# Performance work log

Hardware: AMD Instinct MI355X
Metric: run time of the kernel (lower is better)

## Reference

```python
import jax, jax.numpy as jnp
import numpy as np

# Dims: T=out_seq_len, B=batch, D=hidden_dim, H=hidden_dim_de, E=embedding_size, C=feat_channels
T, B, D, H, E, C, FH, FW = 32, 16, 512, 512, 512, 512, 8, 32


def _lstm_dir(x_seq, W_ih, W_hh, b_ih, b_hh, reverse):
    # x_seq: (T, B, D); PyTorch gate order i, f, g, o
    gx = jnp.einsum('tbd,gd->tbg', x_seq, W_ih) + b_ih  # (T, B, 4H)
    Hh = W_hh.shape[1]
    def step(carry, g_t):
        h, c = carry
        g = g_t + h @ W_hh.T + b_hh
        i, f, gg, o = jnp.split(g, 4, axis=-1)
        c = jax.nn.sigmoid(f) * c + jax.nn.sigmoid(i) * jnp.tanh(gg)
        h = jax.nn.sigmoid(o) * jnp.tanh(c)
        return (h, c), h
    init = (jnp.zeros((x_seq.shape[1], Hh), x_seq.dtype),
            jnp.zeros((x_seq.shape[1], Hh), x_seq.dtype))
    _, hs = jax.lax.scan(step, init, gx, reverse=reverse)
    return hs  # (T, B, H)


def setup_inputs() -> dict:
    key = jax.random.key(0)
    ks = jax.random.split(key, 16)
    s = 0.02
    inp = {
        'hidden_en': jax.random.normal(ks[0], (T, B, D), jnp.float32),
        'conv_f': jax.random.normal(ks[1], (B, C, FH, FW), jnp.float32),
        # bidirectional LSTM params (PyTorch layout: W_ih (4H, D), W_hh (4H, H))
        'W_ih_f': jax.random.normal(ks[2], (4 * H, D), jnp.float32) * s,
        'W_hh_f': jax.random.normal(ks[3], (4 * H, H), jnp.float32) * s,
        'b_ih_f': jnp.zeros((4 * H,), jnp.float32),
        'b_hh_f': jnp.zeros((4 * H,), jnp.float32),
        'W_ih_b': jax.random.normal(ks[4], (4 * H, D), jnp.float32) * s,
        'W_hh_b': jax.random.normal(ks[5], (4 * H, H), jnp.float32) * s,
        'b_ih_b': jnp.zeros((4 * H,), jnp.float32),
        'b_hh_b': jnp.zeros((4 * H,), jnp.float32),
        # linear_decode: (H, 2H)
        'W_dec': jax.random.normal(ks[6], (H, 2 * H), jnp.float32) * s,
        'b_dec': jnp.zeros((H,), jnp.float32),
        # conv_em: 3x3, C -> E (OIHW)
        'W_em': jax.random.normal(ks[7], (E, C, 3, 3), jnp.float32) * s,
        'b_em': jnp.zeros((E,), jnp.float32),
        # attention h_em: 1x1 conv == linear H -> E
        'W_hem': jax.random.normal(ks[8], (E, H), jnp.float32) * s,
        'b_hem': jnp.zeros((E,), jnp.float32),
        # conv_att: 1x1 conv E -> 1
        'w_att': jax.random.normal(ks[9], (E,), jnp.float32) * s,
        'b_att': jnp.zeros((), jnp.float32),
    }
    return inp


def reference(hidden_en, conv_f, W_ih_f, W_hh_f, b_ih_f, b_hh_f,
              W_ih_b, W_hh_b, b_ih_b, b_hh_b, W_dec, b_dec,
              W_em, b_em, W_hem, b_hem, w_att, b_att):
    # decoder_ctc: bidirectional LSTM + linear
    h_fwd = _lstm_dir(hidden_en, W_ih_f, W_hh_f, b_ih_f, b_hh_f, reverse=False)
    h_bwd = _lstm_dir(hidden_en, W_ih_b, W_hh_b, b_ih_b, b_hh_b, reverse=True)
    hidden_de = jnp.concatenate([h_fwd, h_bwd], axis=-1) @ W_dec.T + b_dec  # (T, B, H)

    # conv_em: 3x3 same-padding conv, NCHW
    x_em = jax.lax.conv_general_dilated(
        conv_f, W_em, window_strides=(1, 1), padding='SAME',
        dimension_numbers=('NCHW', 'OIHW', 'NCHW')) + b_em[None, :, None, None]  # (B,E,FH,FW)
    att_x_em = jnp.transpose(x_em.reshape(x_em.shape[0], E, -1), (0, 2, 1))  # (B, HW, E)

    # batched attention over all timesteps (dropout is identity at eval)
    h_em = jnp.einsum('tbh,eh->tbe', hidden_de, W_hem) + b_hem  # (T, B, E)
    feat = jnp.tanh(x_em[None] + h_em[:, :, :, None, None])     # (T, B, E, FH, FW)
    scores = jnp.einsum('tbehw,e->tbhw', feat, w_att) + b_att   # (T, B, FH, FW)
    alpha = jax.nn.softmax(scores.reshape(scores.shape[0], scores.shape[1], -1), axis=-1)  # (T,B,HW)
    att = jnp.einsum('tbn,bne->tbe', alpha, att_x_em)           # (T, B, E)

    ctc_out = jnp.concatenate([hidden_de, att], axis=-1)        # (T, B, H+E)
    return jnp.transpose(ctc_out, (1, 0, 2))                    # (B, T, H+E)
```

## Files before the change

### kernel.cpp

```cpp
#include <hip/hip_runtime.h>
#include <hip/hip_bf16.h>
#include <math.h>

#define T_LEN 32
#define BATCH 16
#define DDIM  512
#define HDIM  512
#define EDIM  512
#define CDIM  512
#define FHH   8
#define FWW   32
#define HW    256
#define G4    2048
#define PADH  10
#define PADW  34
#define WLP   520

typedef __attribute__((ext_vector_type(8))) short bf16x8;
typedef __attribute__((ext_vector_type(4))) float f32x4;

__device__ __forceinline__ ushort bfr(float x) {
    union { float f; uint32_t u; } c; c.f = x;
    uint32_t r = (c.u + 0x7FFFu + ((c.u >> 16) & 1u)) >> 16;
    return (ushort)r;
}

__device__ __forceinline__ float frcp(float x) { return __builtin_amdgcn_rcpf(x); }
__device__ __forceinline__ float ftanh(float x) {
    return 1.f - 2.f * frcp(1.f + __expf(2.f * x));
}
__device__ __forceinline__ float fsig(float x) {
    return frcp(1.f + __expf(-x));
}

__device__ __forceinline__ void ld_lds16(const void* g, void* l) {
    __builtin_amdgcn_global_load_lds((const __attribute__((address_space(1))) void*)g,
                                     (__attribute__((address_space(3))) void*)l, 16, 0, 0);
}

__device__ __forceinline__ void st_u16_sc1(ushort* p, ushort v) {
    asm volatile("global_store_short %0, %1, off sc1" :: "v"(p), "v"((uint)v) : "memory");
}
__device__ __forceinline__ void st_i32_sc1(int* p, int v) {
    asm volatile("global_store_dword %0, %1, off sc1" :: "v"(p), "v"(v) : "memory");
}
__device__ __forceinline__ void st_f32_sc1(float* p, float v) {
    asm volatile("global_store_dword %0, %1, off sc1" :: "v"(p), "v"(v) : "memory");
}
__device__ __forceinline__ int ld_i32_sc1(const int* p) {
    int v;
    asm volatile("global_load_dword %0, %1, off sc1\n\ts_waitcnt vmcnt(0)"
                 : "=v"(v) : "v"(p) : "memory");
    return v;
}

struct PrepArgs { const float* s[7]; ushort* d[7]; };
__global__ __launch_bounds__(256) void prep_all(
    PrepArgs a, int* __restrict__ syncbuf,
    const float* __restrict__ conv_f, ushort* __restrict__ padT,
    const float* __restrict__ W_em, ushort* __restrict__ Wt)
{
    __shared__ float tile[32][33];
    const int bid = blockIdx.x, tid = threadIdx.x;
    if (bid < 5120) {
        int i = bid * 256 + tid;
        if (i < 80) st_i32_sc1(syncbuf + i, 0);
        const int e0 = 65536, e1 = 327680, e2 = 589824, e3 = 851968,
                  e4 = 1114112, e5 = 1245184;
        int seg, base;
        if      (i < e0) { seg = 0; base = 0;  }
        else if (i < e1) { seg = 1; base = e0; }
        else if (i < e2) { seg = 2; base = e1; }
        else if (i < e3) { seg = 3; base = e2; }
        else if (i < e4) { seg = 4; base = e3; }
        else if (i < e5) { seg = 5; base = e4; }
        else             { seg = 6; base = e5; }
        int li = i - base;
        float4 v = ((const float4*)a.s[seg])[li];
        ushort4 o;
        o.x = bfr(v.x); o.y = bfr(v.y); o.z = bfr(v.z); o.w = bfr(v.w);
        ((ushort4*)a.d[seg])[li] = o;
        return;
    }
    if (bid < 7168) {
        int id = bid - 5120;
        int s0 = (id & 7) * 32, c0 = ((id >> 3) & 15) * 32, b = id >> 7;
        int lo = tid & 31, hi = tid >> 5;
#pragma unroll
        for (int it = 0; it < 4; ++it) {
            int cl = hi + it * 8;
            tile[cl][lo] = conv_f[((size_t)(b * CDIM + c0 + cl)) * HW + s0 + lo];
        }
        __syncthreads();
#pragma unroll
        for (int it = 0; it < 4; ++it) {
            int sl = hi + it * 8;
            int s = s0 + sl;
            int y = s >> 5, x = s & 31;
            padT[(((size_t)b * PADH + y + 1) * PADW + (x + 1)) * CDIM + c0 + lo] =
                bfr(tile[lo][sl]);
        }
        return;
    }
    if (bid < 7840) {
        int gid = (bid - 7168) * 256 + tid;
        int c4 = gid & 127;
        int cellb = gid >> 7;
        int cell = cellb % 84;
        int b = cellb / 84;
        int y, x;
        if (cell < 34) { y = 0; x = cell; }
        else if (cell < 68) { y = 9; x = cell - 34; }
        else { int k2 = cell - 68; y = 1 + (k2 >> 1); x = (k2 & 1) ? 33 : 0; }
        ((ushort4*)padT)[(((size_t)b * PADH + y) * PADW + x) * (CDIM / 4) + c4] =
            make_ushort4(0, 0, 0, 0);
        return;
    }
    {
        int gid = (bid - 7840) * 256 + tid;
        int c = gid % CDIM;
        int t = gid / CDIM;
        int e = t % EDIM;
        int tap = t / EDIM;
        int dy = tap / 3, dx = tap % 3;
        Wt[gid] = bfr(W_em[((e * CDIM + c) * 3 + dy) * 3 + dx]);
    }
}

__device__ __forceinline__ void tile64_compute(
    const ushort* Ap0, const ushort* Bp0, int K,
    ushort* smem, int tid, f32x4 (&acc)[2][2])
{
    ushort* As = smem;
    ushort* Bs = smem + 2048;
    const int w = tid >> 6, lane = tid & 63;
    ushort* AsW = &As[w * 512];
    ushort* BsW = &Bs[w * 512];
    const int wm = (w >> 1) * 32, wn = (w & 1) * 32;
    const int kb = (lane >> 4) * 8, fr = lane & 15;
    for (int kk = 0; kk < K; kk += 32) {
        __syncthreads();
        ld_lds16(Ap0 + kk, AsW);
        ld_lds16(Bp0 + kk, BsW);
        __syncthreads();
        bf16x8 af[2], bg[2];
#pragma unroll
        for (int i = 0; i < 2; ++i)
            af[i] = *(const bf16x8*)&As[(wm + i * 16 + fr) * 32 + kb];
#pragma unroll
        for (int j = 0; j < 2; ++j)
            bg[j] = *(const bf16x8*)&Bs[(wn + j * 16 + fr) * 32 + kb];
#pragma unroll
        for (int i = 0; i < 2; ++i)
#pragma unroll
            for (int j = 0; j < 2; ++j)
                acc[i][j] = __builtin_amdgcn_mfma_f32_16x16x32_bf16(af[i], bg[j], acc[i][j], 0, 0, 0);
    }
}

__global__ __launch_bounds__(256) void gemm64(
    const ushort* __restrict__ A, const ushort* __restrict__ B,
    const float* __restrict__ bias0,
    float* __restrict__ C, ushort* __restrict__ Cbf, float* __restrict__ Cscat,
    int M, int N, int K)
{
    __shared__ ushort smem[4096];
    const int n0 = blockIdx.x * 64, m0 = blockIdx.y * 64;
    const int tid = threadIdx.x, w = tid >> 6, lane = tid & 63;
    const int r0 = tid >> 2, c0 = (tid & 3) * 8;
    f32x4 acc[2][2];
#pragma unroll
    for (int i = 0; i < 2; ++i)
#pragma unroll
        for (int j = 0; j < 2; ++j) acc[i][j] = {0.f, 0.f, 0.f, 0.f};
    tile64_compute(A + (size_t)(m0 + r0) * K + c0, B + (size_t)(n0 + r0) * K + c0,
                   K, smem, tid, acc);
    const int wm = (w >> 1) * 32, wn = (w & 1) * 32;
    const int col = lane & 15, rq = (lane >> 4) * 4;
#pragma unroll
    for (int i = 0; i < 2; ++i) {
#pragma unroll
        for (int r = 0; r < 4; ++r) {
            int m = m0 + wm + i * 16 + rq + r;
#pragma unroll
            for (int j = 0; j < 2; ++j) {
                int n = n0 + wn + j * 16 + col;
                float v = acc[i][j][r];
                if (bias0) v += bias0[n];
                if (C)   C[(size_t)m * N + n] = v;
                if (Cbf) Cbf[(size_t)m * N + n] = bfr(v);
                if (Cscat) {
                    int t = m >> 4, b = m & 15;
                    Cscat[((size_t)(b * T_LEN + t)) * 1024 + n] = v;
                }
            }
        }
    }
}

__global__ __launch_bounds__(256) void fused_main(
    const ushort* __restrict__ Whh_f, const ushort* __restrict__ Whh_b,
    float* __restrict__ gx_f, float* __restrict__ gx_b,
    const ushort* __restrict__ hen_bf,
    const ushort* __restrict__ Wih_f, const ushort* __restrict__ Wih_b,
    const float* __restrict__ b_ih_f, const float* __restrict__ b_hh_f,
    const float* __restrict__ b_ih_b, const float* __restrict__ b_hh_b,
    ushort* __restrict__ hs_bf,
    int* __restrict__ syncbuf,
    const ushort* __restrict__ padT, const ushort* __restrict__ Wt,
    const float* __restrict__ bias_em, float* __restrict__ xem)
{
    __shared__ ushort smem[64 * WLP];
    const int bid = blockIdx.x, tid = threadIdx.x;
    const int w = tid >> 6, lane = tid & 63;
    int* flags = syncbuf;
    int* gcnt  = syncbuf + 64;

    if (bid < 64) {
        const int dir = bid >> 5;
        const int j0 = (bid & 31) * 16;
        const ushort* W = dir ? Whh_b : Whh_f;
        const float* gx = dir ? gx_b : gx_f;
#pragma unroll
        for (int i = 0; i < 16; ++i) {
            int row = w * 16 + i;
            int g = row >> 4, jl = row & 15;
            bf16x8 v = *(const bf16x8*)(W + ((size_t)(g * 512 + j0 + jl)) * 512 + lane * 8);
            *(bf16x8*)&smem[row * WLP + lane * 8] = v;
        }
        __syncthreads();
        if (tid >= 64) return;
        __builtin_amdgcn_s_setprio(1);

        const int fr = lane & 15, kq = lane >> 4;
        const int j = j0 + fr;
        const int* fq = &flags[dir * 32 + (lane & 31)];
        f32x4 cr = {0.f, 0.f, 0.f, 0.f};
        int mt_done = -1;
        for (int step = 0; step < T_LEN; ++step) {
            const int tcur = dir ? (T_LEN - 1 - step) : step;
            const int mt = tcur >> 2;
            if (mt != mt_done) {
                const int* gp = &gcnt[dir * 8 + mt];
                for (;;) {
                    int v = ld_i32_sc1(gp);
                    if (v >= 32) break;
                    __builtin_amdgcn_s_sleep(4);
                }
                mt_done = mt;
            }
            float gxv[4][4];
#pragma unroll
            for (int r = 0; r < 4; ++r) {
                const float* gxr = gx + ((size_t)tcur * BATCH + (kq * 4 + r)) * G4 + j;
#pragma unroll
                for (int g = 0; g < 4; ++g)
                    asm volatile("global_load_dword %0, %1, off sc1"
                                 : "=v"(gxv[r][g]) : "v"(gxr + g * 512));
            }
            f32x4 acc[4];
#pragma unroll
            for (int g = 0; g < 4; ++g) acc[g] = {0.f, 0.f, 0.f, 0.f};
            if (step > 0) {
                const int tprev = dir ? tcur + 1 : tcur - 1;
                const ushort* hp = hs_bf + ((size_t)tprev * BATCH + fr) * 1024 + dir * 512 + kq * 8;
                bf16x8 hreg[16];
#pragma unroll
                for (int u = 0; u < 16; ++u)
                    asm volatile("global_load_dwordx4 %0, %1, off sc1"
                                 : "=v"(hreg[u]) : "v"(hp + u * 32));
                asm volatile("s_waitcnt vmcnt(0)" ::: "memory");
                __builtin_amdgcn_sched_barrier(0);
#pragma unroll
                for (int u = 0; u < 16; ++u) {
#pragma unroll
                    for (int g = 0; g < 4; ++g) {
                        bf16x8 bb = *(const bf16x8*)&smem[(g * 16 + fr) * WLP + kq * 8 + u * 32];
                        acc[g] = __builtin_amdgcn_mfma_f32_16x16x32_bf16(hreg[u], bb, acc[g], 0, 0, 0);
                    }
                }
            } else {
                asm volatile("s_waitcnt vmcnt(0)" ::: "memory");
                __builtin_amdgcn_sched_barrier(0);
            }
#pragma unroll
            for (int r = 0; r < 4; ++r) {
                int b = kq * 4 + r;
                float gi = gxv[r][0] + acc[0][r];
                float gf = gxv[r][1] + acc[1][r];
                float gg = gxv[r][2] + acc[2][r];
                float go = gxv[r][3] + acc[3][r];
                float si = fsig(gi), sf = fsig(gf), so = fsig(go);
                float c = sf * cr[r] + si * ftanh(gg);
                cr[r] = c;
                float h = so * ftanh(c);
                st_u16_sc1(hs_bf + ((size_t)tcur * BATCH + b) * 1024 + dir * 512 + j, bfr(h));
            }
            if (step < T_LEN - 1) {
                asm volatile("s_waitcnt vmcnt(0)" ::: "memory");
                if (lane == 0) st_i32_sc1(&flags[bid], step + 1);
                const int need = step + 1;
                for (;;) {
                    int v = ld_i32_sc1(fq);
                    if (__all(v >= need)) break;
                    __builtin_amdgcn_s_sleep(1);
                }
            }
        }
        return;
    }

    if (bid < 576) {
        const int gi = bid - 64;
        const int dir = gi & 1;
        const int q = gi >> 1;
        const int nt = q & 31;
        const int mt0 = q >> 5;
        const int mtile = dir ? (7 - mt0) : mt0;
        const ushort* Bw = dir ? Wih_b : Wih_f;
        const float* bi0 = dir ? b_ih_b : b_ih_f;
        const float* bi1 = dir ? b_hh_b : b_hh_f;
        float* Cg = dir ? gx_b : gx_f;
        const int m0 = mtile * 64, n0 = nt * 64;
        const int r0 = tid >> 2, c0 = (tid & 3) * 8;
        f32x4 acc[2][2];
#pragma unroll
        for (int i = 0; i < 2; ++i)
#pragma unroll
            for (int j = 0; j < 2; ++j) acc[i][j] = {0.f, 0.f, 0.f, 0.f};
        tile64_compute(hen_bf + (size_t)(m0 + r0) * 512 + c0,
                       Bw + (size_t)(n0 + r0) * 512 + c0, 512, smem, tid, acc);
        const int wm = (w >> 1) * 32, wn = (w & 1) * 32;
        const int col = lane & 15, rq = (lane >> 4) * 4;
#pragma unroll
        for (int i = 0; i < 2; ++i)
#pragma unroll
            for (int r = 0; r < 4; ++r) {
                int m = m0 + wm + i * 16 + rq + r;
#pragma unroll
                for (int j2 = 0; j2 < 2; ++j2) {
                    int n = n0 + wn + j2 * 16 + col;
                    st_f32_sc1(&Cg[(size_t)m * G4 + n], acc[i][j2][r] + bi0[n] + bi1[n]);
                }
            }
        asm volatile("s_waitcnt vmcnt(0)" ::: "memory");
        __syncthreads();
        if (tid == 0) atomicAdd(&gcnt[dir * 8 + mtile], 1);
        return;
    }

    {
        const int cbid = bid - 576;
        const int n0 = (cbid & 7) * 64, m0 = (cbid >> 3) * 64;
        const int r0 = tid >> 2, c0 = (tid & 3) * 8;
        const int b = m0 >> 8, s0 = m0 & 255, y0 = s0 >> 5;
        const int y = y0 + (r0 >> 5), x = r0 & 31;
        const ushort* Abase = padT + (((size_t)b * PADH + y) * PADW + x) * CDIM + c0;
        const ushort* Bbase = Wt + (size_t)(n0 + r0) * CDIM + c0;
        f32x4 acc[2][2];
#pragma unroll
        for (int i = 0; i < 2; ++i)
#pragma unroll
            for (int j = 0; j < 2; ++j) acc[i][j] = {0.f, 0.f, 0.f, 0.f};
        for (int tap = 0; tap < 9; ++tap) {
            const int dy = tap / 3, dx = tap % 3;
            tile64_compute(Abase + ((size_t)dy * PADW + dx) * CDIM,
                           Bbase + (size_t)tap * EDIM * CDIM, 512, smem, tid, acc);
        }
        const int wm = (w >> 1) * 32, wn = (w & 1) * 32;
        const int col = lane & 15, rq = (lane >> 4) * 4;
#pragma unroll
        for (int i = 0; i < 2; ++i)
#pragma unroll
            for (int r = 0; r < 4; ++r) {
                int m = m0 + wm + i * 16 + rq + r;
                int s = m & 255;
#pragma unroll
                for (int j2 = 0; j2 < 2; ++j2) {
                    int e = n0 + wn + j2 * 16 + col;
                    xem[((size_t)b * EDIM + e) * HW + s] = acc[i][j2][r] + bias_em[e];
                }
            }
    }
}

__global__ __launch_bounds__(256) void attention(
    const float* __restrict__ xem,
    const float* __restrict__ hem,
    const float* __restrict__ watt,
    float* __restrict__ out) {
    int i = blockIdx.x;
    int k = i >> 3;
    int b = ((i & 7) << 1) | (k & 1);
    int t = k >> 1;
    int tb = t * 16 + b;
    int tid = threadIdx.x;
    __shared__ float hl[512], wl[512], al[256], red[8];
    for (int q = tid; q < 512; q += 256) { hl[q] = hem[(size_t)tb * 512 + q]; wl[q] = watt[q]; }
    __syncthreads();
    const float* xb = xem + (size_t)b * EDIM * HW;
    float sc = 0.f;
#pragma unroll 4
    for (int e = 0; e < 512; ++e)
        sc += ftanh(xb[(size_t)e * HW + tid] + hl[e]) * wl[e];
    float m = sc;
#pragma unroll
    for (int o = 32; o; o >>= 1) m = fmaxf(m, __shfl_xor(m, o));
    if ((tid & 63) == 0) red[tid >> 6] = m;
    __syncthreads();
    m = fmaxf(fmaxf(red[0], red[1]), fmaxf(red[2], red[3]));
    float ex = __expf(sc - m);
    float s = ex;
#pragma unroll
    for (int o = 32; o; o >>= 1) s += __shfl_xor(s, o);
    if ((tid & 63) == 0) red[4 + (tid >> 6)] = s;
    __syncthreads();
    s = red[4] + red[5] + red[6] + red[7];
    al[tid] = ex * frcp(s);
    __syncthreads();
    float* ob = out + ((size_t)(b * T_LEN + t)) * 1024 + 512;
    for (int eo = 0; eo < 512; eo += 256) {
        int e = eo + tid;
        const float* xr = xb + (size_t)e * HW;
        float acc = 0.f;
#pragma unroll 4
        for (int n = 0; n < 256; n += 4) {
            float4 v = *(const float4*)&xr[n];
            acc += al[n] * v.x + al[n + 1] * v.y + al[n + 2] * v.z + al[n + 3] * v.w;
        }
        ob[e] = acc;
    }
}

extern "C" void kernel_launch(void* const* d_in, const int* in_sizes, int n_in,
                              void* d_out, int out_size, void* d_ws, size_t ws_size,
                              hipStream_t stream) {
    const float* hidden_en = (const float*)d_in[0];
    const float* conv_f    = (const float*)d_in[1];
    const float* W_ih_f    = (const float*)d_in[2];
    const float* W_hh_f    = (const float*)d_in[3];
    const float* b_ih_f    = (const float*)d_in[4];
    const float* b_hh_f    = (const float*)d_in[5];
    const float* W_ih_b    = (const float*)d_in[6];
    const float* W_hh_b    = (const float*)d_in[7];
    const float* b_ih_b    = (const float*)d_in[8];
    const float* b_hh_b    = (const float*)d_in[9];
    const float* W_dec     = (const float*)d_in[10];
    const float* b_dec     = (const float*)d_in[11];
    const float* W_em      = (const float*)d_in[12];
    const float* b_em      = (const float*)d_in[13];
    const float* W_hem     = (const float*)d_in[14];
    const float* b_hem     = (const float*)d_in[15];
    const float* w_att     = (const float*)d_in[16];
    float* out = (float*)d_out;

    char* p = (char*)d_ws;
    auto alloc = [&](size_t bytes) { void* r = p; p += (bytes + 255) & ~(size_t)255; return r; };
    float*    gx_f    = (float*)alloc((size_t)T_LEN * BATCH * G4 * 4);
    float*    gx_b    = (float*)alloc((size_t)T_LEN * BATCH * G4 * 4);
    float*    h_em    = (float*)alloc((size_t)T_LEN * BATCH * 512 * 4);
    float*    x_em    = (float*)alloc((size_t)BATCH * EDIM * HW * 4);
    ushort*   padT    = (ushort*)alloc((size_t)BATCH * PADH * PADW * CDIM * 2);
    ushort*   Wt      = (ushort*)alloc((size_t)9 * EDIM * CDIM * 2);
    ushort*   hen_bf  = (ushort*)alloc((size_t)T_LEN * BATCH * DDIM * 2);
    ushort*   Wihf_bf = (ushort*)alloc((size_t)G4 * DDIM * 2);
    ushort*   Wihb_bf = (ushort*)alloc((size_t)G4 * DDIM * 2);
    ushort*   Whhf_bf = (ushort*)alloc((size_t)G4 * HDIM * 2);
    ushort*   Whhb_bf = (ushort*)alloc((size_t)G4 * HDIM * 2);
    ushort*   Wdec_bf = (ushort*)alloc((size_t)HDIM * 1024 * 2);
    ushort*   Whem_bf = (ushort*)alloc((size_t)EDIM * HDIM * 2);
    ushort*   hs_bf   = (ushort*)alloc((size_t)T_LEN * BATCH * 1024 * 2);
    ushort*   hde_bf  = (ushort*)alloc((size_t)T_LEN * BATCH * 512 * 2);
    int*      syncbuf = (int*)alloc(512);

    PrepArgs pa;
    pa.s[0] = hidden_en; pa.d[0] = hen_bf;
    pa.s[1] = W_ih_f;    pa.d[1] = Wihf_bf;
    pa.s[2] = W_ih_b;    pa.d[2] = Wihb_bf;
    pa.s[3] = W_hh_f;    pa.d[3] = Whhf_bf;
    pa.s[4] = W_hh_b;    pa.d[4] = Whhb_bf;
    pa.s[5] = W_dec;     pa.d[5] = Wdec_bf;
    pa.s[6] = W_hem;     pa.d[6] = Whem_bf;
    prep_all<<<17056, 256, 0, stream>>>(pa, syncbuf, conv_f, padT, W_em, Wt);

    fused_main<<<1088, 256, 0, stream>>>(Whhf_bf, Whhb_bf, gx_f, gx_b, hen_bf,
                                         Wihf_bf, Wihb_bf, b_ih_f, b_hh_f,
                                         b_ih_b, b_hh_b, hs_bf, syncbuf,
                                         padT, Wt, b_em, x_em);

    gemm64<<<dim3(8, 8), 256, 0, stream>>>(hs_bf, Wdec_bf, b_dec,
                                           nullptr, hde_bf, out, 512, 512, 1024);

    gemm64<<<dim3(8, 8), 256, 0, stream>>>(hde_bf, Whem_bf, b_hem,
                                           h_em, nullptr, nullptr, 512, 512, 512);

    attention<<<512, 256, 0, stream>>>(x_em, h_em, w_att, out);
}
```

Baseline: 253.1 us.

## Interleave gate inputs, prefetch next step's gx, batch flag polling, restage conv weight prep

The input-projection GEMM now stores gx with the four gates interleaved per hidden unit, so each recurrent lane fetches its gates for a timestep with one dwordx4 load. The load for the next timestep is issued right after the current step finishes, overlapping it with the inter-block flag wait. The flag wait is also moved to the start of the step and reads four flags per vectorized load. Separately, the conv weight transpose in prep is restructured to one block per output channel, with coalesced reads staged through LDS, which cuts the prep grid size. The costs are extra registers and a changed sync order that must keep the gx readiness checks correct.

```diff
diff --git a/kernel.cpp b/kernel.cpp
--- a/kernel.cpp
+++ b/kernel.cpp
@@ -18,6 +18,7 @@
 
 typedef __attribute__((ext_vector_type(8))) short bf16x8;
 typedef __attribute__((ext_vector_type(4))) float f32x4;
+typedef __attribute__((ext_vector_type(4))) int i32x4;
 
 __device__ __forceinline__ ushort bfr(float x) {
     union { float f; uint32_t u; } c; c.f = x;
@@ -51,6 +52,17 @@
     int v;
     asm volatile("global_load_dword %0, %1, off sc1\n\ts_waitcnt vmcnt(0)"
                  : "=v"(v) : "v"(p) : "memory");
+    return v;
+}
+__device__ __forceinline__ i32x4 ld_i32x4_sc1(const int* p) {
+    i32x4 v;
+    asm volatile("global_load_dwordx4 %0, %1, off sc1\n\ts_waitcnt vmcnt(0)"
+                 : "=v"(v) : "v"(p) : "memory");
+    return v;
+}
+__device__ __forceinline__ f32x4 ld_f32x4_sc1_async(const float* p) {
+    f32x4 v;
+    asm volatile("global_load_dwordx4 %0, %1, off sc1" : "=v"(v) : "v"(p));
     return v;
 }
 
@@ -61,10 +73,11 @@
     const float* __restrict__ W_em, ushort* __restrict__ Wt)
 {
     __shared__ float tile[32][33];
+    __shared__ ushort lt[9 * 512];
     const int bid = blockIdx.x, tid = threadIdx.x;
     if (bid < 5120) {
         int i = bid * 256 + tid;
-        if (i < 80) st_i32_sc1(syncbuf + i, 0);
+        if (i < 128) st_i32_sc1(syncbuf + i, 0);
         const int e0 = 65536, e1 = 327680, e2 = 589824, e3 = 851968,
                   e4 = 1114112, e5 = 1245184;
         int seg, base;
@@ -117,13 +130,23 @@
         return;
     }
     {
-        int gid = (bid - 7840) * 256 + tid;
-        int c = gid % CDIM;
-        int t = gid / CDIM;
-        int e = t % EDIM;
-        int tap = t / EDIM;
-        int dy = tap / 3, dx = tap % 3;
-        Wt[gid] = bfr(W_em[((e * CDIM + c) * 3 + dy) * 3 + dx]);
+        const int e = bid - 7840;
+        const float4* src = (const float4*)(W_em + (size_t)e * 4608);
+        for (int k = tid; k < 1152; k += 256) {
+            float4 v = src[k];
+            int base = k * 4;
+#pragma unroll
+            for (int j = 0; j < 4; ++j) {
+                int idx = base + j;
+                int c = idx / 9, tap = idx % 9;
+                lt[tap * 512 + c] = bfr(((const float*)&v)[j]);
+            }
+        }
+        __syncthreads();
+        for (int k = tid; k < 1152; k += 256) {
+            int tap = k >> 7, c4 = k & 127;
+            ((ushort4*)(Wt + ((size_t)tap * EDIM + e) * CDIM))[c4] = ((ushort4*)lt)[k];
+        }
     }
 }
 
@@ -200,7 +223,7 @@
 
 __global__ __launch_bounds__(256) void fused_main(
     const ushort* __restrict__ Whh_f, const ushort* __restrict__ Whh_b,
-    float* __restrict__ gx_f, float* __restrict__ gx_b,
+    float* __restrict__ gxT_f, float* __restrict__ gxT_b,
     const ushort* __restrict__ hen_bf,
     const ushort* __restrict__ Wih_f, const ushort* __restrict__ Wih_b,
     const float* __restrict__ b_ih_f, const float* __restrict__ b_hh_f,
@@ -220,7 +243,7 @@
         const int dir = bid >> 5;
         const int j0 = (bid & 31) * 16;
         const ushort* W = dir ? Whh_b : Whh_f;
-        const float* gx = dir ? gx_b : gx_f;
+        const float* gx = dir ? gxT_b : gxT_f;
 #pragma unroll
         for (int i = 0; i < 16; ++i) {
             int row = w * 16 + i;
@@ -234,29 +257,28 @@
 
         const int fr = lane & 15, kq = lane >> 4;
         const int j = j0 + fr;
-        const int* fq = &flags[dir * 32 + (lane & 31)];
+        const int* fq4 = &flags[dir * 32 + (lane & 7) * 4];
+        const int t0 = dir ? (T_LEN - 1) : 0;
+        int mt_ok = t0 >> 2;
+        {
+            const int* gp = &gcnt[dir * 8 + mt_ok];
+            while (ld_i32_sc1(gp) < 32) __builtin_amdgcn_s_sleep(4);
+        }
+        f32x4 gq[4];
+#pragma unroll
+        for (int r = 0; r < 4; ++r)
+            gq[r] = ld_f32x4_sc1_async(gx + (((size_t)t0 * BATCH + kq * 4 + r) * 512 + j) * 4);
         f32x4 cr = {0.f, 0.f, 0.f, 0.f};
-        int mt_done = -1;
         for (int step = 0; step < T_LEN; ++step) {
             const int tcur = dir ? (T_LEN - 1 - step) : step;
-            const int mt = tcur >> 2;
-            if (mt != mt_done) {
-                const int* gp = &gcnt[dir * 8 + mt];
+            if (step > 0) {
+                const int need = step;
                 for (;;) {
-                    int v = ld_i32_sc1(gp);
-                    if (v >= 32) break;
-                    __builtin_amdgcn_s_sleep(4);
+                    i32x4 v = ld_i32x4_sc1(fq4);
+                    int mn = min(min(v[0], v[1]), min(v[2], v[3]));
+                    if (__all(mn >= need)) break;
+                    __builtin_amdgcn_s_sleep(1);
                 }
-                mt_done = mt;
-            }
-            float gxv[4][4];
-#pragma unroll
-            for (int r = 0; r < 4; ++r) {
-                const float* gxr = gx + ((size_t)tcur * BATCH + (kq * 4 + r)) * G4 + j;
-#pragma unroll
-                for (int g = 0; g < 4; ++g)
-                    asm volatile("global_load_dword %0, %1, off sc1"
-                                 : "=v"(gxv[r][g]) : "v"(gxr + g * 512));
             }
             f32x4 acc[4];
 #pragma unroll
@@ -286,10 +308,10 @@
 #pragma unroll
             for (int r = 0; r < 4; ++r) {
                 int b = kq * 4 + r;
-                float gi = gxv[r][0] + acc[0][r];
-                float gf = gxv[r][1] + acc[1][r];
-                float gg = gxv[r][2] + acc[2][r];
-                float go = gxv[r][3] + acc[3][r];
+                float gi = gq[r][0] + acc[0][r];
+                float gf = gq[r][1] + acc[1][r];
+                float gg = gq[r][2] + acc[2][r];
+                float go = gq[r][3] + acc[3][r];
                 float si = fsig(gi), sf = fsig(gf), so = fsig(go);
                 float c = sf * cr[r] + si * ftanh(gg);
                 cr[r] = c;
@@ -299,16 +321,29 @@
             if (step < T_LEN - 1) {
                 asm volatile("s_waitcnt vmcnt(0)" ::: "memory");
                 if (lane == 0) st_i32_sc1(&flags[bid], step + 1);
-                const int need = step + 1;
-                for (;;) {
-                    int v = ld_i32_sc1(fq);
-                    if (__all(v >= need)) break;
-                    __builtin_amdgcn_s_sleep(1);
+                const int tnext = dir ? tcur - 1 : tcur + 1;
+                const int mtn = tnext >> 2;
+                if (mtn != mt_ok) {
+                    const int* gp = &gcnt[dir * 8 + mtn];
+                    while (ld_i32_sc1(gp) < 32) __builtin_amdgcn_s_sleep(2);
+                    mt_ok = mtn;
                 }
+#pragma unroll
+                for (int r = 0; r < 4; ++r)
+                    gq[r] = ld_f32x4_sc1_async(gx + (((size_t)tnext * BATCH + kq * 4 + r) * 512 + j) * 4);
             }
         }
         return;
     }
+
+    const int r0 = tid >> 2, c0 = (tid & 3) * 8;
+    const int wm = (w >> 1) * 32, wn = (w & 1) * 32;
+    const int col = lane & 15, rq = (lane >> 4) * 4;
+    f32x4 acc[2][2];
+#pragma unroll
+    for (int i = 0; i < 2; ++i)
+#pragma unroll
+        for (int j = 0; j < 2; ++j) acc[i][j] = {0.f, 0.f, 0.f, 0.f};
 
     if (bid < 576) {
         const int gi = bid - 64;
@@ -320,18 +355,10 @@
         const ushort* Bw = dir ? Wih_b : Wih_f;
         const float* bi0 = dir ? b_ih_b : b_ih_f;
         const float* bi1 = dir ? b_hh_b : b_hh_f;
-        float* Cg = dir ? gx_b : gx_f;
+        float* Cg = dir ? gxT_b : gxT_f;
         const int m0 = mtile * 64, n0 = nt * 64;
-        const int r0 = tid >> 2, c0 = (tid & 3) * 8;
-        f32x4 acc[2][2];
-#pragma unroll
-        for (int i = 0; i < 2; ++i)
-#pragma unroll
-            for (int j = 0; j < 2; ++j) acc[i][j] = {0.f, 0.f, 0.f, 0.f};
         tile64_compute(hen_bf + (size_t)(m0 + r0) * 512 + c0,
                        Bw + (size_t)(n0 + r0) * 512 + c0, 512, smem, tid, acc);
-        const int wm = (w >> 1) * 32, wn = (w & 1) * 32;
-        const int col = lane & 15, rq = (lane >> 4) * 4;
 #pragma unroll
         for (int i = 0; i < 2; ++i)
 #pragma unroll
@@ -340,7 +367,8 @@
 #pragma unroll
                 for (int j2 = 0; j2 < 2; ++j2) {
                     int n = n0 + wn + j2 * 16 + col;
-                    st_f32_sc1(&Cg[(size_t)m * G4 + n], acc[i][j2][r] + bi0[n] + bi1[n]);
+                    st_f32_sc1(&Cg[(size_t)m * G4 + (n & 511) * 4 + (n >> 9)],
+                               acc[i][j2][r] + bi0[n] + bi1[n]);
                 }
             }
         asm volatile("s_waitcnt vmcnt(0)" ::: "memory");
@@ -348,27 +376,18 @@
         if (tid == 0) atomicAdd(&gcnt[dir * 8 + mtile], 1);
         return;
     }
-
     {
         const int cbid = bid - 576;
         const int n0 = (cbid & 7) * 64, m0 = (cbid >> 3) * 64;
-        const int r0 = tid >> 2, c0 = (tid & 3) * 8;
         const int b = m0 >> 8, s0 = m0 & 255, y0 = s0 >> 5;
         const int y = y0 + (r0 >> 5), x = r0 & 31;
         const ushort* Abase = padT + (((size_t)b * PADH + y) * PADW + x) * CDIM + c0;
         const ushort* Bbase = Wt + (size_t)(n0 + r0) * CDIM + c0;
-        f32x4 acc[2][2];
-#pragma unroll
-        for (int i = 0; i < 2; ++i)
-#pragma unroll
-            for (int j = 0; j < 2; ++j) acc[i][j] = {0.f, 0.f, 0.f, 0.f};
         for (int tap = 0; tap < 9; ++tap) {
             const int dy = tap / 3, dx = tap % 3;
             tile64_compute(Abase + ((size_t)dy * PADW + dx) * CDIM,
                            Bbase + (size_t)tap * EDIM * CDIM, 512, smem, tid, acc);
         }
-        const int wm = (w >> 1) * 32, wn = (w & 1) * 32;
-        const int col = lane & 15, rq = (lane >> 4) * 4;
 #pragma unroll
         for (int i = 0; i < 2; ++i)
 #pragma unroll
@@ -456,8 +475,8 @@
 
     char* p = (char*)d_ws;
     auto alloc = [&](size_t bytes) { void* r = p; p += (bytes + 255) & ~(size_t)255; return r; };
-    float*    gx_f    = (float*)alloc((size_t)T_LEN * BATCH * G4 * 4);
-    float*    gx_b    = (float*)alloc((size_t)T_LEN * BATCH * G4 * 4);
+    float*    gxT_f   = (float*)alloc((size_t)T_LEN * BATCH * G4 * 4);
+    float*    gxT_b   = (float*)alloc((size_t)T_LEN * BATCH * G4 * 4);
     float*    h_em    = (float*)alloc((size_t)T_LEN * BATCH * 512 * 4);
     float*    x_em    = (float*)alloc((size_t)BATCH * EDIM * HW * 4);
     ushort*   padT    = (ushort*)alloc((size_t)BATCH * PADH * PADW * CDIM * 2);
@@ -471,7 +490,7 @@
     ushort*   Whem_bf = (ushort*)alloc((size_t)EDIM * HDIM * 2);
     ushort*   hs_bf   = (ushort*)alloc((size_t)T_LEN * BATCH * 1024 * 2);
     ushort*   hde_bf  = (ushort*)alloc((size_t)T_LEN * BATCH * 512 * 2);
-    int*      syncbuf = (int*)alloc(512);
+    int*      syncbuf = (int*)alloc(1024);
 
     PrepArgs pa;
     pa.s[0] = hidden_en; pa.d[0] = hen_bf;
@@ -481,9 +500,9 @@
     pa.s[4] = W_hh_b;    pa.d[4] = Whhb_bf;
     pa.s[5] = W_dec;     pa.d[5] = Wdec_bf;
     pa.s[6] = W_hem;     pa.d[6] = Whem_bf;
-    prep_all<<<17056, 256, 0, stream>>>(pa, syncbuf, conv_f, padT, W_em, Wt);
-
-    fused_main<<<1088, 256, 0, stream>>>(Whhf_bf, Whhb_bf, gx_f, gx_b, hen_bf,
+    prep_all<<<8352, 256, 0, stream>>>(pa, syncbuf, conv_f, padT, W_em, Wt);
+
+    fused_main<<<1088, 256, 0, stream>>>(Whhf_bf, Whhb_bf, gxT_f, gxT_b, hen_bf,
                                          Wihf_bf, Wihb_bf, b_ih_f, b_hh_f,
                                          b_ih_b, b_hh_b, hs_bf, syncbuf,
                                          padT, Wt, b_em, x_em);
```

Result: slower. 264.8 us (+4.6%).
